# Performance work log

Hardware: AMD Instinct MI355X
Metric: run time of the kernel (lower is better)

Reference implementation:

```python
import jax, jax.numpy as jnp
import numpy as np

B, S, H, NH, HD, V = 2, 2048, 1024, 16, 64, 32000
BASE = 10000.0
NEG = jnp.finfo(jnp.float32).min


def setup_inputs() -> dict:
    key = jax.random.key(0)
    ks = jax.random.split(key, 12)
    batch = jax.random.randint(ks[0], (B, S), 0, V)
    positions = jnp.broadcast_to(jnp.arange(S), (B, S))
    lengths = jax.random.randint(ks[1], (B,), 1, S + 1)  # >=1 to avoid fully-masked rows
    sc = 1.0 / np.sqrt(H)
    emb = jax.random.normal(ks[2], (V, H), dtype=jnp.float32) * 0.02
    wq = jax.random.normal(ks[3], (H, NH * HD), dtype=jnp.float32) * sc
    bq = jnp.zeros((NH * HD,), jnp.float32)
    wk = jax.random.normal(ks[4], (H, NH * HD), dtype=jnp.float32) * sc
    bk = jnp.zeros((NH * HD,), jnp.float32)
    wv = jax.random.normal(ks[5], (H, NH * HD), dtype=jnp.float32) * sc
    bv = jnp.zeros((NH * HD,), jnp.float32)
    wo = jax.random.normal(ks[6], (NH * HD, H), dtype=jnp.float32) * sc
    bo = jnp.zeros((H,), jnp.float32)
    return dict(batch=batch, positions=positions, lengths=lengths, emb=emb,
                wq=wq, bq=bq, wk=wk, bk=bk, wv=wv, bv=bv, wo=wo, bo=bo)


def _rope(x, positions):
    # x: [B, NH, S, HD]; positions: [B, S] int
    inv_freq = 1.0 / (BASE ** (jnp.arange(0, HD, 2, dtype=jnp.float32) / HD))  # [HD/2]
    freqs = positions.astype(jnp.float32)[..., None] * inv_freq               # [B, S, HD/2]
    ang = jnp.concatenate([freqs, freqs], axis=-1)                            # [B, S, HD]
    cos = jnp.cos(ang)[:, None]                                               # [B, 1, S, HD]
    sin = jnp.sin(ang)[:, None]
    x1, x2 = x[..., :HD // 2], x[..., HD // 2:]
    rot = jnp.concatenate([-x2, x1], axis=-1)
    return x * cos + rot * sin


def reference(batch, positions, lengths, emb, wq, bq, wk, bk, wv, bv, wo, bo):
    h = emb[batch]                                                 # [B, S, H]
    q = (h @ wq + bq).reshape(B, S, NH, HD).transpose(0, 2, 1, 3)  # [B, NH, S, HD]
    k = (h @ wk + bk).reshape(B, S, NH, HD).transpose(0, 2, 1, 3)
    v = (h @ wv + bv).reshape(B, S, NH, HD).transpose(0, 2, 1, 3)
    q = _rope(q, positions)
    k = _rope(k, positions)
    scores = jnp.einsum('bhqd,bhkd->bhqk', q, k) / np.sqrt(HD)     # [B, NH, S, S]
    causal = jnp.triu(jnp.full((S, S), NEG, jnp.float32), 1)
    pad = jnp.where(jnp.arange(S)[None, :] < lengths[:, None], 0.0, NEG)  # [B, S]
    mask = pad[:, None, None, :] + causal[None, None]              # [B, 1, S, S]
    attn = jax.nn.softmax(scores + mask, axis=-1)
    out = jnp.einsum('bhqk,bhkd->bhqd', attn, v)                   # [B, NH, S, HD]
    out = out.transpose(0, 2, 1, 3).reshape(B, S, NH * HD)
    return out @ wo + bo                                           # [B, S, H]
```

## Files before the change

kernel.cpp:

```cpp
#include <hip/hip_runtime.h>
#include <hip/hip_bf16.h>
#include <cstdint>

#define DEVINL __device__ __forceinline__

typedef __attribute__((ext_vector_type(8))) short short8;
typedef __attribute__((ext_vector_type(4))) float f32x4;

constexpr int B_ = 2, S_ = 2048, H_ = 1024, NH_ = 16, HD_ = 64;
constexpr int M_ = B_ * S_;
constexpr float SC2 = 0.18033688f;

DEVINL float bf2f(unsigned short h) {
    unsigned u = ((unsigned)h) << 16;
    float f; __builtin_memcpy(&f, &u, 4); return f;
}
DEVINL unsigned short f2bf(float f) {
    unsigned u; __builtin_memcpy(&u, &f, 4);
    u += 0x7FFFu + ((u >> 16) & 1u);
    return (unsigned short)(u >> 16);
}
DEVINL unsigned pk2bf(float a, float b) {
    __hip_bfloat162 h = __float22bfloat162_rn(float2{a, b});
    unsigned u; __builtin_memcpy(&u, &h, 4); return u;
}
DEVINL float fexp2(float x) {
#if __has_builtin(__builtin_amdgcn_exp2f)
    return __builtin_amdgcn_exp2f(x);
#else
    return exp2f(x);
#endif
}
DEVINL float ldin(const void* p, size_t i, int fp32) {
    return fp32 ? ((const float*)p)[i] : bf2f(((const unsigned short*)p)[i]);
}
DEVINL void gl16(const void* g, void* l) {
    __builtin_amdgcn_global_load_lds(
        (const __attribute__((address_space(1))) unsigned int*)g,
        (__attribute__((address_space(3))) unsigned int*)l, 16, 0, 0);
}
DEVINL f32x4 mfma16(short8 a, short8 b, f32x4 c) {
    return __builtin_amdgcn_mfma_f32_16x16x32_bf16(a, b, c, 0, 0, 0);
}
DEVINL void fsincos(float rev01, float* sn, float* cs) {
#if __has_builtin(__builtin_amdgcn_sinf) && __has_builtin(__builtin_amdgcn_cosf)
    *sn = __builtin_amdgcn_sinf(rev01);
    *cs = __builtin_amdgcn_cosf(rev01);
#else
    float a = rev01 * 6.28318530717958647692f;
    *sn = __sinf(a); *cs = __cosf(a);
#endif
}
DEVINL int detect_fp32(const unsigned short* emb, int t) {
    unsigned short hw = emb[2 * t];
    unsigned e = (hw >> 7) & 0xFFu;
    int s = (((e >= 90u) && (e <= 126u)) || ((hw & 0x7FFFu) == 0u)) ? 1 : 0;
    #pragma unroll
    for (int o = 1; o < 64; o <<= 1) s += __shfl_xor(s, o);
    __shared__ int cnt[4];
    if ((t & 63) == 0) cnt[t >> 6] = s;
    __syncthreads();
    return ((cnt[0] + cnt[1] + cnt[2] + cnt[3]) > 192) ? 0 : 1;
}

__global__ __launch_bounds__(256) void k_prep(const void* w0, const void* w1,
                                              const void* w2, const void* w3,
                                              const void* bq, const void* bk,
                                              const void* bv, const void* bo,
                                              const unsigned short* __restrict__ emb,
                                              const int* __restrict__ batch,
                                              int* __restrict__ flag,
                                              float* __restrict__ biasws,
                                              unsigned short* __restrict__ wT,
                                              unsigned short* __restrict__ hbuf) {
    int tx = threadIdx.x, ty = threadIdx.y, t = ty * 32 + tx;
    int fp32 = detect_fp32(emb, t);
    int z = blockIdx.z;
    if (z == 4) {
        if (!fp32) return;
        int g = blockIdx.y * 32 + blockIdx.x;
        int w = t >> 6, lane = t & 63;
        int row = g * 4 + w;
        int tok = batch[row];
        const float4* s = (const float4*)((const float*)emb + (size_t)tok * H_);
        unsigned long long* d = (unsigned long long*)(hbuf + (size_t)row * H_);
        #pragma unroll
        for (int c = 0; c < 4; c++) {
            float4 x = s[lane + 64 * c];
            d[lane + 64 * c] = (unsigned long long)f2bf(x.x)
                             | ((unsigned long long)f2bf(x.y) << 16)
                             | ((unsigned long long)f2bf(x.z) << 32)
                             | ((unsigned long long)f2bf(x.w) << 48);
        }
        return;
    }
    __shared__ float tile[32][33];
    int mat = z;
    if (mat == 0 && blockIdx.y == 0) {
        if (blockIdx.x == 0 && t == 0) flag[0] = fp32;
        if (blockIdx.x < 16) {
            int i = blockIdx.x * 256 + t;
            const void* src = (i < 1024) ? bq : (i < 2048) ? bk : (i < 3072) ? bv : bo;
            biasws[i] = ldin(src, (size_t)(i & 1023), fp32);
        }
    }
    const void* w = (mat == 0) ? w0 : (mat == 1) ? w1 : (mat == 2) ? w2 : w3;
    int n0 = blockIdx.x * 32, k0 = blockIdx.y * 32;
    for (int i = ty; i < 32; i += 8)
        tile[i][tx] = ldin(w, (size_t)(k0 + i) * 1024 + n0 + tx, fp32);
    __syncthreads();
    unsigned short* dst = wT + (size_t)mat * 1024 * 1024;
    for (int i = ty; i < 32; i += 8)
        dst[(size_t)(n0 + i) * 1024 + k0 + tx] = f2bf(tile[tx][i]);
}

__global__ __launch_bounds__(256) void k_gemm_qkv(const unsigned short* __restrict__ embb,
                                                  const unsigned short* __restrict__ hbuf,
                                                  const int* __restrict__ batch,
                                                  const unsigned short* __restrict__ Bt,
                                                  const float* __restrict__ bias,
                                                  const int* __restrict__ positions,
                                                  const int* __restrict__ flag,
                                                  unsigned short* __restrict__ qo,
                                                  unsigned short* __restrict__ ko,
                                                  unsigned short* __restrict__ vt) {
    constexpr int K = 1024;
    __shared__ alignas(16) unsigned short As[2][128 * 32];
    __shared__ alignas(16) unsigned short Bs[2][128 * 32];
    int t = threadIdx.x, lane = t & 63, quad = lane >> 4, n16 = lane & 15;
    int w = t >> 6, wm = w >> 1, wn = w & 1;
    int m0 = blockIdx.y * 128, n0 = blockIdx.x * 128;
    int fp32 = flag[0];
    int r0 = t >> 2, r1 = 64 + r0;
    int ka = (t & 3) * 8;
    const unsigned short* a0;
    const unsigned short* a1;
    if (fp32) {
        a0 = hbuf + (size_t)(m0 + r0) * K;
        a1 = hbuf + (size_t)(m0 + r1) * K;
    } else {
        a0 = embb + (size_t)batch[m0 + r0] * K;
        a1 = embb + (size_t)batch[m0 + r1] * K;
    }
    const unsigned short* b0 = Bt + (size_t)(n0 + r0) * K;
    const unsigned short* b1 = Bt + (size_t)(n0 + r1) * K;
    f32x4 acc[4][4];
    #pragma unroll
    for (int mi = 0; mi < 4; mi++)
        #pragma unroll
        for (int ni = 0; ni < 4; ni++) acc[mi][ni] = (f32x4){0.f, 0.f, 0.f, 0.f};
    for (int k0 = 0; k0 < K; k0 += 64) {
        __syncthreads();
        gl16(a0 + k0 + ka,      &As[0][t * 8]);
        gl16(a1 + k0 + ka,      &As[0][(t + 256) * 8]);
        gl16(a0 + k0 + 32 + ka, &As[1][t * 8]);
        gl16(a1 + k0 + 32 + ka, &As[1][(t + 256) * 8]);
        gl16(b0 + k0 + ka,      &Bs[0][t * 8]);
        gl16(b1 + k0 + ka,      &Bs[0][(t + 256) * 8]);
        gl16(b0 + k0 + 32 + ka, &Bs[1][t * 8]);
        gl16(b1 + k0 + 32 + ka, &Bs[1][(t + 256) * 8]);
        __syncthreads();
        #pragma unroll
        for (int ks = 0; ks < 2; ks++) {
            short8 af[4], bfr[4];
            #pragma unroll
            for (int mi = 0; mi < 4; mi++)
                af[mi] = *(const short8*)&As[ks][(wm * 64 + mi * 16 + n16) * 32 + quad * 8];
            #pragma unroll
            for (int ni = 0; ni < 4; ni++)
                bfr[ni] = *(const short8*)&Bs[ks][(wn * 64 + ni * 16 + n16) * 32 + quad * 8];
            #pragma unroll
            for (int mi = 0; mi < 4; mi++)
                #pragma unroll
                for (int ni = 0; ni < 4; ni++)
                    acc[mi][ni] = mfma16(af[mi], bfr[ni], acc[mi][ni]);
        }
    }
    int colbase = n0 + wn * 64;
    int buf = colbase >> 10;
    int cc = colbase & 1023;
    float bb[4];
    #pragma unroll
    for (int ni = 0; ni < 4; ni++) bb[ni] = bias[colbase + ni * 16 + n16];
    if (buf == 2) {
        #pragma unroll
        for (int mi = 0; mi < 4; mi++) {
            int row = m0 + wm * 64 + mi * 16 + quad * 4;
            int bb_ = row >> 11;
            int s0 = row & 2047;
            int pos = (s0 & ~31) + quad * 8 + (mi & 1) * 4;
            #pragma unroll
            for (int ni = 0; ni < 4; ni++) {
                int f = cc + ni * 16 + n16;
                unsigned long long pk =
                      (unsigned long long)pk2bf(acc[mi][ni][0] + bb[ni], acc[mi][ni][1] + bb[ni])
                    | ((unsigned long long)pk2bf(acc[mi][ni][2] + bb[ni], acc[mi][ni][3] + bb[ni]) << 32);
                *(unsigned long long*)(vt + ((size_t)(bb_ * 1024 + f)) * 2048 + pos) = pk;
            }
        }
    } else {
        unsigned short* out = (buf == 0) ? qo : ko;
        float osc = (buf == 0) ? SC2 : 1.0f;
        float revf[2];
        #pragma unroll
        for (int ni = 0; ni < 2; ni++) {
            float d = (float)(ni * 16 + n16);
            revf[ni] = __expf(d * -0.28782313f) * 0.15915494f;
        }
        #pragma unroll
        for (int mi = 0; mi < 4; mi++) {
            int row0 = m0 + wm * 64 + mi * 16 + quad * 4;
            #pragma unroll
            for (int i = 0; i < 4; i++) {
                int row = row0 + i;
                float pos = (float)positions[row];
                #pragma unroll
                for (int ni = 0; ni < 2; ni++) {
                    float rev = pos * revf[ni];
                    float fr = rev - floorf(rev);
                    float sn, cs; fsincos(fr, &sn, &cs);
                    float x1 = (acc[mi][ni][i] + bb[ni]) * osc;
                    float x2 = (acc[mi][ni + 2][i] + bb[ni + 2]) * osc;
                    out[(size_t)row * 1024 + cc + ni * 16 + n16] = f2bf(x1 * cs - x2 * sn);
                    out[(size_t)row * 1024 + cc + (ni + 2) * 16 + n16] = f2bf(x2 * cs + x1 * sn);
                }
            }
        }
    }
}

__global__ __launch_bounds__(256) void k_attn(const unsigned short* __restrict__ q,
                                              const unsigned short* __restrict__ k_,
                                              const unsigned short* __restrict__ vt,
                                              const int* __restrict__ lengths,
                                              unsigned short* __restrict__ o) {
    __shared__ alignas(16) unsigned short Ks[2][64 * 64];
    __shared__ alignas(16) unsigned short Vs[2][64 * 64];
    int bx = blockIdx.x;
    int jraw = bx & 15, hh = (bx >> 4) & 15, b = bx >> 8;
    int j = (b & 1) ? (15 - jraw) : jraw;
    int t = threadIdx.x, w = t >> 6, lane = t & 63, quad = lane >> 4, n16 = lane & 15;
    int len = lengths[b];
    int tile0 = j, tile1 = 31 - j;
    int kend0 = min(tile0 * 64 + 64, len);
    int kend1 = min(tile1 * 64 + 64, len);
    int nkt = (kend1 + 63) >> 6;
    int qrow0 = tile0 * 64 + w * 16 + n16;
    int qrow1 = tile1 * 64 + w * 16 + n16;
    int limit0 = min(qrow0, len - 1);
    int limit1 = min(qrow1, len - 1);
    int tbw0 = tile0 * 64 + w * 16;
    int tbw1 = tile1 * 64 + w * 16;
    short8 qf[2][2];
    {
        size_t qa = ((size_t)(b * S_ + qrow0)) * H_ + hh * 64 + quad * 8;
        size_t qb2 = ((size_t)(b * S_ + qrow1)) * H_ + hh * 64 + quad * 8;
        qf[0][0] = *(const short8*)(q + qa);  qf[0][1] = *(const short8*)(q + qa + 32);
        qf[1][0] = *(const short8*)(q + qb2); qf[1][1] = *(const short8*)(q + qb2 + 32);
    }
    f32x4 oa[2][4];
    float l_[2] = {0.f, 0.f};
    #pragma unroll
    for (int s = 0; s < 2; s++)
        #pragma unroll
        for (int nb = 0; nb < 4; nb++) oa[s][nb] = (f32x4){0.f, 0.f, 0.f, 0.f};
    const unsigned short* kbase = k_ + ((size_t)b * S_) * H_ + hh * 64;
    const unsigned short* vbase = vt + ((size_t)(b * 1024 + hh * 64)) * 2048;
    int sr0 = t >> 3, sc0 = (t & 7) ^ (sr0 & 7);
    int sr1 = (t + 256) >> 3, sc1 = (t & 7) ^ (sr1 & 7);
    auto stage = [&](int kt) {
        int kb = kt * 64, bi = kt & 1;
        gl16(kbase + (size_t)(kb + sr0) * H_ + sc0 * 8, &Ks[bi][t * 8]);
        gl16(kbase + (size_t)(kb + sr1) * H_ + sc1 * 8, &Ks[bi][(t + 256) * 8]);
        gl16(vbase + (size_t)sr0 * 2048 + kb + sc0 * 8, &Vs[bi][t * 8]);
        gl16(vbase + (size_t)sr1 * 2048 + kb + sc1 * 8, &Vs[bi][(t + 256) * 8]);
    };
    stage(0);
    for (int kt = 0; kt < nkt; kt++) {
        int kb = kt * 64, bi = kt & 1;
        __syncthreads();
        if (kt + 1 < nkt) stage(kt + 1);
        const unsigned short* Kb = Ks[bi];
        const unsigned short* Vb = Vs[bi];
        short8 kf[4][2];
        #pragma unroll
        for (int st = 0; st < 4; st++)
            #pragma unroll
            for (int hf = 0; hf < 2; hf++) {
                int ky = st * 16 + n16;
                kf[st][hf] = *(const short8*)&Kb[ky * 64 + (((hf * 4 + quad) ^ (ky & 7)) * 8)];
            }
        short8 vf[2][4];
        #pragma unroll
        for (int p = 0; p < 2; p++)
            #pragma unroll
            for (int nb = 0; nb < 4; nb++) {
                int f = nb * 16 + n16;
                vf[p][nb] = *(const short8*)&Vb[f * 64 + (((p * 4 + quad) ^ (f & 7)) * 8)];
            }
        #pragma unroll
        for (int si = 0; si < 2; si++) {
            if (si == 0 && kb >= kend0) continue;
            int limit = si ? limit1 : limit0;
            int tbw = si ? tbw1 : tbw0;
            f32x4 sc[4];
            #pragma unroll
            for (int st = 0; st < 4; st++) {
                f32x4 z = (f32x4){0.f, 0.f, 0.f, 0.f};
                z = mfma16(kf[st][0], qf[si][0], z);
                z = mfma16(kf[st][1], qf[si][1], z);
                sc[st] = z;
            }
            float rs = 0.f;
            if (kb + 64 <= min(tbw, len)) {
                #pragma unroll
                for (int st = 0; st < 4; st++)
                    #pragma unroll
                    for (int i = 0; i < 4; i++) {
                        float p = fexp2(sc[st][i]);
                        rs += p;
                        sc[st][i] = p;
                    }
            } else {
                #pragma unroll
                for (int st = 0; st < 4; st++)
                    #pragma unroll
                    for (int i = 0; i < 4; i++) {
                        int kg = kb + st * 16 + quad * 4 + i;
                        float p = (kg <= limit) ? fexp2(sc[st][i]) : 0.f;
                        rs += p;
                        sc[st][i] = p;
                    }
            }
            rs += __shfl_xor(rs, 16);
            rs += __shfl_xor(rs, 32);
            l_[si] += rs;
            #pragma unroll
            for (int p = 0; p < 2; p++) {
                union { unsigned u[4]; short8 v8; } pp;
                pp.u[0] = pk2bf(sc[2 * p][0], sc[2 * p][1]);
                pp.u[1] = pk2bf(sc[2 * p][2], sc[2 * p][3]);
                pp.u[2] = pk2bf(sc[2 * p + 1][0], sc[2 * p + 1][1]);
                pp.u[3] = pk2bf(sc[2 * p + 1][2], sc[2 * p + 1][3]);
                #pragma unroll
                for (int nb = 0; nb < 4; nb++)
                    oa[si][nb] = mfma16(pp.v8, vf[p][nb], oa[si][nb]);
            }
        }
    }
    #pragma unroll
    for (int si = 0; si < 2; si++) {
        int tb = si ? tile1 : tile0;
        f32x4 rl;
        #pragma unroll
        for (int i = 0; i < 4; i++) rl[i] = 1.f / __shfl(l_[si], quad * 4 + i);
        #pragma unroll
        for (int nb = 0; nb < 4; nb++) {
            #pragma unroll
            for (int i = 0; i < 4; i++) {
                int row = tb * 64 + w * 16 + quad * 4 + i;
                o[((size_t)(b * S_ + row)) * H_ + hh * 64 + nb * 16 + n16] =
                    f2bf(oa[si][nb][i] * rl[i]);
            }
        }
    }
}

__global__ __launch_bounds__(256) void k_gemm64(const unsigned short* __restrict__ A,
                                                const unsigned short* __restrict__ Bt,
                                                const float* __restrict__ bias,
                                                unsigned short* __restrict__ Cb,
                                                float* __restrict__ Cf,
                                                const int* __restrict__ flag) {
    constexpr int K = 1024, N = 1024;
    __shared__ alignas(16) unsigned short As[2][64 * 32];
    __shared__ alignas(16) unsigned short Bs[2][128 * 32];
    int t = threadIdx.x, lane = t & 63, quad = lane >> 4, n16 = lane & 15;
    int w = t >> 6, wm = w & 1, wn = w >> 1;
    int m0 = blockIdx.y * 64, n0 = blockIdx.x * 128;
    int r0 = t >> 2, r1 = 64 + r0, ka = (t & 3) * 8;
    const unsigned short* a0 = A + (size_t)(m0 + r0) * K;
    const unsigned short* b0 = Bt + (size_t)(n0 + r0) * K;
    const unsigned short* b1 = Bt + (size_t)(n0 + r1) * K;
    f32x4 acc[2][4];
    #pragma unroll
    for (int mi = 0; mi < 2; mi++)
        #pragma unroll
        for (int ni = 0; ni < 4; ni++) acc[mi][ni] = (f32x4){0.f, 0.f, 0.f, 0.f};
    for (int k0 = 0; k0 < K; k0 += 64) {
        __syncthreads();
        gl16(a0 + k0 + ka,      &As[0][t * 8]);
        gl16(a0 + k0 + 32 + ka, &As[1][t * 8]);
        gl16(b0 + k0 + ka,      &Bs[0][t * 8]);
        gl16(b1 + k0 + ka,      &Bs[0][(t + 256) * 8]);
        gl16(b0 + k0 + 32 + ka, &Bs[1][t * 8]);
        gl16(b1 + k0 + 32 + ka, &Bs[1][(t + 256) * 8]);
        __syncthreads();
        #pragma unroll
        for (int ks = 0; ks < 2; ks++) {
            short8 af[2], bfr[4];
            #pragma unroll
            for (int mi = 0; mi < 2; mi++)
                af[mi] = *(const short8*)&As[ks][(wm * 32 + mi * 16 + n16) * 32 + quad * 8];
            #pragma unroll
            for (int ni = 0; ni < 4; ni++)
                bfr[ni] = *(const short8*)&Bs[ks][(wn * 64 + ni * 16 + n16) * 32 + quad * 8];
            #pragma unroll
            for (int mi = 0; mi < 2; mi++)
                #pragma unroll
                for (int ni = 0; ni < 4; ni++)
                    acc[mi][ni] = mfma16(af[mi], bfr[ni], acc[mi][ni]);
        }
    }
    int fp32out = (flag[0] == 1);
    #pragma unroll
    for (int mi = 0; mi < 2; mi++) {
        #pragma unroll
        for (int ni = 0; ni < 4; ni++) {
            int row = m0 + wm * 32 + mi * 16 + quad * 4;
            int col = n0 + wn * 64 + ni * 16 + n16;
            float bb = bias[col];
            #pragma unroll
            for (int i = 0; i < 4; i++) {
                float val = acc[mi][ni][i] + bb;
                size_t idx = (size_t)(row + i) * N + col;
                if (fp32out) Cf[idx] = val;
                else         Cb[idx] = f2bf(val);
            }
        }
    }
}

extern "C" void kernel_launch(void* const* d_in, const int* in_sizes, int n_in,
                              void* d_out, int out_size, void* d_ws, size_t ws_size,
                              hipStream_t stream) {
    (void)in_sizes; (void)n_in; (void)out_size; (void)ws_size;
    const int* batch     = (const int*)d_in[0];
    const int* positions = (const int*)d_in[1];
    const int* lengths   = (const int*)d_in[2];
    const void* emb = d_in[3];
    const void* wq = d_in[4];  const void* bq = d_in[5];
    const void* wk = d_in[6];  const void* bk = d_in[7];
    const void* wv = d_in[8];  const void* bv = d_in[9];
    const void* wo = d_in[10]; const void* bo = d_in[11];

    char* ws = (char*)d_ws;
    int*   flag   = (int*)ws;
    float* biasws = (float*)(ws + 4096);
    unsigned short* wT = (unsigned short*)(ws + 20480);
    size_t off = 20480 + (8ull << 20);
    unsigned short* hbuf = (unsigned short*)(ws + off); off += (8ull << 20);
    unsigned short* qb   = (unsigned short*)(ws + off); off += (8ull << 20);
    unsigned short* kb2  = (unsigned short*)(ws + off); off += (8ull << 20);
    unsigned short* vtb  = (unsigned short*)(ws + off); off += (8ull << 20);
    unsigned short* ao   = (unsigned short*)(ws + off); off += (8ull << 20);

    k_prep<<<dim3(32, 32, 5), dim3(32, 8), 0, stream>>>(
        wq, wk, wv, wo, bq, bk, bv, bo, (const unsigned short*)emb, batch,
        flag, biasws, wT, hbuf);

    k_gemm_qkv<<<dim3(3072 / 128, M_ / 128), 256, 0, stream>>>(
        (const unsigned short*)emb, hbuf, batch, wT, biasws, positions, flag,
        qb, kb2, vtb);

    k_attn<<<B_ * NH_ * 16, 256, 0, stream>>>(qb, kb2, vtb, lengths, ao);

    k_gemm64<<<dim3(1024 / 128, M_ / 64), 256, 0, stream>>>(
        ao, wT + (3ull << 20), biasws + 3072,
        (unsigned short*)d_out, (float*)d_out, flag);
}
```

Before: 300.0 us.

## Split paired causal query tiles into one tile per attention block

The attention kernel previously had each block process two query tiles (j and 31-j) to balance causal work, sharing K/V staging between them. Now each block handles a single 64-row query tile, doubling the grid to 1024 blocks and using a reversed tile order on alternating heads for balance. This raises parallelism and lowers per-thread register use, at the cost of loading K/V tiles from global memory roughly twice as often and less balanced per-block work.

```diff
diff --git a/kernel.cpp b/kernel.cpp
--- a/kernel.cpp
+++ b/kernel.cpp
@@ -237,33 +237,25 @@
     __shared__ alignas(16) unsigned short Ks[2][64 * 64];
     __shared__ alignas(16) unsigned short Vs[2][64 * 64];
     int bx = blockIdx.x;
-    int jraw = bx & 15, hh = (bx >> 4) & 15, b = bx >> 8;
-    int j = (b & 1) ? (15 - jraw) : jraw;
+    int traw = bx & 31, hh = (bx >> 5) & 15, b = bx >> 9;
+    int tile = ((bx >> 8) & 1) ? (31 - traw) : traw;
     int t = threadIdx.x, w = t >> 6, lane = t & 63, quad = lane >> 4, n16 = lane & 15;
     int len = lengths[b];
-    int tile0 = j, tile1 = 31 - j;
-    int kend0 = min(tile0 * 64 + 64, len);
-    int kend1 = min(tile1 * 64 + 64, len);
-    int nkt = (kend1 + 63) >> 6;
-    int qrow0 = tile0 * 64 + w * 16 + n16;
-    int qrow1 = tile1 * 64 + w * 16 + n16;
-    int limit0 = min(qrow0, len - 1);
-    int limit1 = min(qrow1, len - 1);
-    int tbw0 = tile0 * 64 + w * 16;
-    int tbw1 = tile1 * 64 + w * 16;
-    short8 qf[2][2];
+    int kend = min(tile * 64 + 64, len);
+    int nkt = (kend + 63) >> 6;
+    int qrow = tile * 64 + w * 16 + n16;
+    int limit = min(qrow, len - 1);
+    int tbw = tile * 64 + w * 16;
+    short8 qf[2];
     {
-        size_t qa = ((size_t)(b * S_ + qrow0)) * H_ + hh * 64 + quad * 8;
-        size_t qb2 = ((size_t)(b * S_ + qrow1)) * H_ + hh * 64 + quad * 8;
-        qf[0][0] = *(const short8*)(q + qa);  qf[0][1] = *(const short8*)(q + qa + 32);
-        qf[1][0] = *(const short8*)(q + qb2); qf[1][1] = *(const short8*)(q + qb2 + 32);
-    }
-    f32x4 oa[2][4];
-    float l_[2] = {0.f, 0.f};
-    #pragma unroll
-    for (int s = 0; s < 2; s++)
-        #pragma unroll
-        for (int nb = 0; nb < 4; nb++) oa[s][nb] = (f32x4){0.f, 0.f, 0.f, 0.f};
+        size_t qa = ((size_t)(b * S_ + qrow)) * H_ + hh * 64 + quad * 8;
+        qf[0] = *(const short8*)(q + qa);
+        qf[1] = *(const short8*)(q + qa + 32);
+    }
+    f32x4 oa[4];
+    float l_ = 0.f;
+    #pragma unroll
+    for (int nb = 0; nb < 4; nb++) oa[nb] = (f32x4){0.f, 0.f, 0.f, 0.f};
     const unsigned short* kbase = k_ + ((size_t)b * S_) * H_ + hh * 64;
     const unsigned short* vbase = vt + ((size_t)(b * 1024 + hh * 64)) * 2048;
     int sr0 = t >> 3, sc0 = (t & 7) ^ (sr0 & 7);
@@ -290,6 +282,38 @@
                 int ky = st * 16 + n16;
                 kf[st][hf] = *(const short8*)&Kb[ky * 64 + (((hf * 4 + quad) ^ (ky & 7)) * 8)];
             }
+        f32x4 sc[4];
+        #pragma unroll
+        for (int st = 0; st < 4; st++) {
+            f32x4 z = (f32x4){0.f, 0.f, 0.f, 0.f};
+            z = mfma16(kf[st][0], qf[0], z);
+            z = mfma16(kf[st][1], qf[1], z);
+            sc[st] = z;
+        }
+        float rs = 0.f;
+        if (kb + 64 <= min(tbw, len)) {
+            #pragma unroll
+            for (int st = 0; st < 4; st++)
+                #pragma unroll
+                for (int i = 0; i < 4; i++) {
+                    float p = fexp2(sc[st][i]);
+                    rs += p;
+                    sc[st][i] = p;
+                }
+        } else {
+            #pragma unroll
+            for (int st = 0; st < 4; st++)
+                #pragma unroll
+                for (int i = 0; i < 4; i++) {
+                    int kg = kb + st * 16 + quad * 4 + i;
+                    float p = (kg <= limit) ? fexp2(sc[st][i]) : 0.f;
+                    rs += p;
+                    sc[st][i] = p;
+                }
+        }
+        rs += __shfl_xor(rs, 16);
+        rs += __shfl_xor(rs, 32);
+        l_ += rs;
         short8 vf[2][4];
         #pragma unroll
         for (int p = 0; p < 2; p++)
@@ -299,69 +323,27 @@
                 vf[p][nb] = *(const short8*)&Vb[f * 64 + (((p * 4 + quad) ^ (f & 7)) * 8)];
             }
         #pragma unroll
-        for (int si = 0; si < 2; si++) {
-            if (si == 0 && kb >= kend0) continue;
-            int limit = si ? limit1 : limit0;
-            int tbw = si ? tbw1 : tbw0;
-            f32x4 sc[4];
-            #pragma unroll
-            for (int st = 0; st < 4; st++) {
-                f32x4 z = (f32x4){0.f, 0.f, 0.f, 0.f};
-                z = mfma16(kf[st][0], qf[si][0], z);
-                z = mfma16(kf[st][1], qf[si][1], z);
-                sc[st] = z;
-            }
-            float rs = 0.f;
-            if (kb + 64 <= min(tbw, len)) {
-                #pragma unroll
-                for (int st = 0; st < 4; st++)
-                    #pragma unroll
-                    for (int i = 0; i < 4; i++) {
-                        float p = fexp2(sc[st][i]);
-                        rs += p;
-                        sc[st][i] = p;
-                    }
-            } else {
-                #pragma unroll
-                for (int st = 0; st < 4; st++)
-                    #pragma unroll
-                    for (int i = 0; i < 4; i++) {
-                        int kg = kb + st * 16 + quad * 4 + i;
-                        float p = (kg <= limit) ? fexp2(sc[st][i]) : 0.f;
-                        rs += p;
-                        sc[st][i] = p;
-                    }
-            }
-            rs += __shfl_xor(rs, 16);
-            rs += __shfl_xor(rs, 32);
-            l_[si] += rs;
-            #pragma unroll
-            for (int p = 0; p < 2; p++) {
-                union { unsigned u[4]; short8 v8; } pp;
-                pp.u[0] = pk2bf(sc[2 * p][0], sc[2 * p][1]);
-                pp.u[1] = pk2bf(sc[2 * p][2], sc[2 * p][3]);
-                pp.u[2] = pk2bf(sc[2 * p + 1][0], sc[2 * p + 1][1]);
-                pp.u[3] = pk2bf(sc[2 * p + 1][2], sc[2 * p + 1][3]);
-                #pragma unroll
-                for (int nb = 0; nb < 4; nb++)
-                    oa[si][nb] = mfma16(pp.v8, vf[p][nb], oa[si][nb]);
-            }
-        }
-    }
-    #pragma unroll
-    for (int si = 0; si < 2; si++) {
-        int tb = si ? tile1 : tile0;
-        f32x4 rl;
-        #pragma unroll
-        for (int i = 0; i < 4; i++) rl[i] = 1.f / __shfl(l_[si], quad * 4 + i);
-        #pragma unroll
-        for (int nb = 0; nb < 4; nb++) {
-            #pragma unroll
-            for (int i = 0; i < 4; i++) {
-                int row = tb * 64 + w * 16 + quad * 4 + i;
-                o[((size_t)(b * S_ + row)) * H_ + hh * 64 + nb * 16 + n16] =
-                    f2bf(oa[si][nb][i] * rl[i]);
-            }
+        for (int p = 0; p < 2; p++) {
+            union { unsigned u[4]; short8 v8; } pp;
+            pp.u[0] = pk2bf(sc[2 * p][0], sc[2 * p][1]);
+            pp.u[1] = pk2bf(sc[2 * p][2], sc[2 * p][3]);
+            pp.u[2] = pk2bf(sc[2 * p + 1][0], sc[2 * p + 1][1]);
+            pp.u[3] = pk2bf(sc[2 * p + 1][2], sc[2 * p + 1][3]);
+            #pragma unroll
+            for (int nb = 0; nb < 4; nb++)
+                oa[nb] = mfma16(pp.v8, vf[p][nb], oa[nb]);
+        }
+    }
+    f32x4 rl;
+    #pragma unroll
+    for (int i = 0; i < 4; i++) rl[i] = 1.f / __shfl(l_, quad * 4 + i);
+    #pragma unroll
+    for (int nb = 0; nb < 4; nb++) {
+        #pragma unroll
+        for (int i = 0; i < 4; i++) {
+            int row = tile * 64 + w * 16 + quad * 4 + i;
+            o[((size_t)(b * S_ + row)) * H_ + hh * 64 + nb * 16 + n16] =
+                f2bf(oa[nb][i] * rl[i]);
         }
     }
 }
@@ -463,7 +445,7 @@
         (const unsigned short*)emb, hbuf, batch, wT, biasws, positions, flag,
         qb, kb2, vtb);
 
-    k_attn<<<B_ * NH_ * 16, 256, 0, stream>>>(qb, kb2, vtb, lengths, ao);
+    k_attn<<<B_ * NH_ * 32, 256, 0, stream>>>(qb, kb2, vtb, lengths, ao);
 
     k_gemm64<<<dim3(1024 / 128, M_ / 64), 256, 0, stream>>>(
         ao, wT + (3ull << 20), biasws + 3072,
```

Result: no change. 300.4 us (+0.1%).
